# Kernel tuning notes

Measured on AMD Instinct MI355X. Metric: run time of the kernel, lower is better.

Reference implementation:

```python
import jax, jax.numpy as jnp
import numpy as np

H, HKV, D, HID = 64, 8, 64, 2880
T = 2048
WINDOW = 128
THETA = 150000.0
FACTOR = 32.0
ORIG_MAX = 4096
BETA_FAST, BETA_SLOW = 32.0, 1.0
EPS = 1e-5
SCALE = D ** -0.5
MSCALE = float(0.1 * np.log(FACTOR) + 1.0)  # vLLM YaRN attention mscale


def _yarn_inv_freq():
    # vLLM YaRNScalingRotaryEmbedding inverse frequencies
    def corr_dim(n_rot):
        return D * np.log(ORIG_MAX / (n_rot * 2.0 * np.pi)) / (2.0 * np.log(THETA))
    low = max(int(np.floor(corr_dim(BETA_FAST))), 0)
    high = min(int(np.ceil(corr_dim(BETA_SLOW))), D - 1)
    pow_ = np.arange(0, D, 2, dtype=np.float32) / D
    extrap = 1.0 / (THETA ** pow_)                 # extrapolation inv_freq
    interp = extrap / FACTOR                        # interpolation inv_freq
    ramp = np.clip((np.arange(D // 2, dtype=np.float32) - low) / max(high - low, 1e-3), 0.0, 1.0)
    extrap_mask = 1.0 - ramp
    inv_freq = interp * (1.0 - extrap_mask) + extrap * extrap_mask
    return jnp.asarray(inv_freq, jnp.float32)

_INV_FREQ = _yarn_inv_freq()


def _rope(positions, x):
    # neox-style rotation; x: [T, heads, D]
    freqs = positions.astype(jnp.float32)[:, None] * _INV_FREQ[None, :]  # [T, D/2]
    cos = (jnp.cos(freqs) * MSCALE)[:, None, :]
    sin = (jnp.sin(freqs) * MSCALE)[:, None, :]
    x1, x2 = x[..., : D // 2], x[..., D // 2 :]
    return jnp.concatenate([x1 * cos - x2 * sin, x2 * cos + x1 * sin], axis=-1)


def _attn(q, k, v, sinks):
    # q: [T,H,D]; k,v: [T,HKV,D]; sinks: [H] extra softmax logit per head
    g = H // HKV
    k = jnp.repeat(k, g, axis=1)
    v = jnp.repeat(v, g, axis=1)
    scores = jnp.einsum('qhd,khd->hqk', q, k) * SCALE  # [H,T,T]
    i = jnp.arange(T)[:, None]
    j = jnp.arange(T)[None, :]
    mask = (j <= i) & (i - j < WINDOW)  # causal + sliding window (even layer)
    scores = jnp.where(mask[None], scores, -jnp.inf)
    s = sinks[:, None]                                    # [H,1]
    m = jnp.maximum(jnp.max(scores, axis=-1), s)          # [H,T]
    p = jnp.exp(scores - m[..., None])                    # [H,T,T]
    denom = jnp.sum(p, axis=-1) + jnp.exp(s - m)          # sink adds to denominator only
    out = jnp.einsum('hqk,khd->qhd', p, v) / denom.T[..., None]
    return out.reshape(T, H * D)


def setup_inputs() -> dict:
    key = jax.random.key(0)
    ks = jax.random.split(key, 8)
    return {
        'hidden_states': jax.random.normal(ks[0], (T, HID), jnp.float32),
        'positions': jnp.arange(T, dtype=jnp.int32),
        'norm_w': jnp.ones((HID,), jnp.float32),
        'w_qkv': jax.random.normal(ks[1], ((H + 2 * HKV) * D, HID), jnp.float32) * 0.02,
        'b_qkv': jax.random.normal(ks[2], ((H + 2 * HKV) * D,), jnp.float32) * 0.02,
        'w_o': jax.random.normal(ks[3], (HID, H * D), jnp.float32) * 0.02,
        'b_o': jax.random.normal(ks[4], (HID,), jnp.float32) * 0.02,
        'sinks': jax.random.normal(ks[5], (H,), jnp.float32),
    }


def reference(hidden_states, positions, norm_w, w_qkv, b_qkv, w_o, b_o, sinks):
    x = hidden_states
    t = x * jax.lax.rsqrt(jnp.mean(x * x, axis=-1, keepdims=True) + EPS) * norm_w  # RMSNorm
    qkv = t @ w_qkv.T + b_qkv
    q, k, v = jnp.split(qkv, [H * D, H * D + HKV * D], axis=-1)
    q = _rope(positions, q.reshape(T, H, D))
    k = _rope(positions, k.reshape(T, HKV, D))
    v = v.reshape(T, HKV, D)
    attn_out = _attn(q, k, v, sinks)
    out = attn_out @ w_o.T + b_o
    return out + x  # residual
```

## Files before the change

### kernel.cpp

```cpp
#include <hip/hip_runtime.h>
#include <hip/hip_bf16.h>
#include <stdint.h>

typedef __attribute__((ext_vector_type(8))) short bf16x8;
typedef __attribute__((ext_vector_type(4))) float f32x4;
typedef __attribute__((ext_vector_type(4))) unsigned short u16x4;

#define T_SEQ 2048
#define HID_D 2880
#define KPAD 2944
#define NH 64
#define NKV 8
#define HD 64
#define QKV_N 5120
#define ATT_N 4096
#define WIN 128
#define RSCALE 0.125f
#define MSCALE 1.3465735903f

__device__ __forceinline__ unsigned short f2bf(float f) {
  union { float f; unsigned u; } v; v.f = f;
  unsigned r = v.u + 0x7fffu + ((v.u >> 16) & 1u);
  return (unsigned short)(r >> 16);
}

__device__ __forceinline__ void gload_lds16(const void* g, void* l) {
  __builtin_amdgcn_global_load_lds((const __attribute__((address_space(1))) char*)g,
                                   (__attribute__((address_space(3))) char*)l, 16, 0, 0);
}

__global__ __launch_bounds__(256) void rmsnorm_kernel(const float* __restrict__ x,
                                                      const float* __restrict__ w,
                                                      unsigned short* __restrict__ t_bf) {
  int row = blockIdx.x;
  const float4* xr4 = (const float4*)(x + (size_t)row * HID_D);
  const float4* w4 = (const float4*)w;
  float ss = 0.f;
  for (int i = threadIdx.x; i < 720; i += 256) {
    float4 v = xr4[i];
    ss += v.x * v.x + v.y * v.y + v.z * v.z + v.w * v.w;
  }
  __shared__ float red[256];
  red[threadIdx.x] = ss;
  __syncthreads();
  for (int s = 128; s > 0; s >>= 1) {
    if (threadIdx.x < s) red[threadIdx.x] += red[threadIdx.x + s];
    __syncthreads();
  }
  float rs = rsqrtf(red[0] / (float)HID_D + 1e-5f);
  u16x4* ob = (u16x4*)(t_bf + (size_t)row * KPAD);
  for (int i = threadIdx.x; i < 736; i += 256) {
    u16x4 o = {0, 0, 0, 0};
    if (i < 720) {
      float4 v = xr4[i];
      float4 g = w4[i];
      o = { f2bf(v.x * rs * g.x), f2bf(v.y * rs * g.y),
            f2bf(v.z * rs * g.z), f2bf(v.w * rs * g.w) };
    }
    ob[i] = o;
  }
}

__global__ __launch_bounds__(256) void f2bf_pad_kernel(const float* __restrict__ in,
                                                       unsigned short* __restrict__ out,
                                                       int rows, int in4, int out4) {
  int i = blockIdx.x * 256 + threadIdx.x;
  if (i >= rows * out4) return;
  int c4 = i % out4, row = i / out4;
  u16x4 o = {0, 0, 0, 0};
  if (c4 < in4) {
    float4 v = ((const float4*)(in + (size_t)row * in4 * 4))[c4];
    o = { f2bf(v.x), f2bf(v.y), f2bf(v.z), f2bf(v.w) };
  }
  ((u16x4*)out)[(size_t)row * out4 + c4] = o;
}

template <bool NCHECK, bool PARTIAL>
__global__ __launch_bounds__(512, 2) void gemm256p(const unsigned short* __restrict__ A,
                                                   const unsigned short* __restrict__ B,
                                                   float* __restrict__ C,
                                                   const float* __restrict__ bias,
                                                   int M, int N, int ld, int nt,
                                                   int nbx, int nbxy, int nstore) {
  __shared__ unsigned short sA[2 * 2 * 128 * 64];
  __shared__ unsigned short sB[2 * 2 * 128 * 64];

  const int tid = threadIdx.x;
  const int lane = tid & 63, wid = tid >> 6;
  const int wr = wid >> 2, wc = wid & 3;
  const int lq = lane & 15, ro = lane >> 4;

  const int cpx = gridDim.x >> 3;
  const int swz = (blockIdx.x & 7) * cpx + (blockIdx.x >> 3);
  const int kslice = swz / nbxy;
  const int rem = swz - kslice * nbxy;
  const int bx = rem % nbx, by = rem / nbx;
  const int m0 = by * 256, n0 = bx * 256;

  const unsigned short* Ab = A + (size_t)kslice * nt * 64;
  const unsigned short* Bb = B + (size_t)kslice * nt * 64;
  float* Cb = C + (size_t)kslice * M * nstore;

  const int R0 = tid >> 3;
  const int g0 = (((tid & 7) ^ (R0 & 7)) << 3);
  const size_t aOff = (size_t)(m0 + R0) * ld + g0;
  size_t bOff[2][2];
#pragma unroll
  for (int h = 0; h < 2; ++h)
#pragma unroll
    for (int r = 0; r < 2; ++r) {
      int rr = n0 + h * 128 + r * 64 + R0;
      if (NCHECK) rr = min(rr, N - 1);
      bOff[h][r] = (size_t)rr * ld + g0;
    }

  const int ck0 = ((ro ^ (lq & 7)) << 3);
  const int ck1 = (((4 + ro) ^ (lq & 7)) << 3);

#define STG_A(BUF, H, KT)                                                        \
  { unsigned short* _d = sA + ((BUF) * 2 + (H)) * 8192 + wid * 512;              \
    const unsigned short* _s = Ab + aOff + (size_t)((H) * 128) * ld + (KT) * 64; \
    gload_lds16(_s, _d); gload_lds16(_s + (size_t)64 * ld, _d + 4096); }
#define STG_B(BUF, H, KT)                                                        \
  { unsigned short* _d = sB + ((BUF) * 2 + (H)) * 8192 + wid * 512;              \
    gload_lds16(Bb + bOff[H][0] + (KT) * 64, _d);                                \
    gload_lds16(Bb + bOff[H][1] + (KT) * 64, _d + 4096); }

  bf16x8 aR[8];
  bf16x8 bR0[4], bR1[4];
  f32x4 acc[8][4] = {};

#define LDA(BUF, S)                                                                        \
  { _Pragma("unroll") for (int ii = 0; ii < 4; ++ii) {                                     \
      const int _r = ((BUF) * 2 + wr) * 8192 + ((S) * 64 + ii * 16 + lq) * 64;             \
      aR[ii * 2 + 0] = *(const bf16x8*)&sA[_r + ck0];                                      \
      aR[ii * 2 + 1] = *(const bf16x8*)&sA[_r + ck1]; } }
#define LDB(BUF, NHF, DST)                                                                 \
  { _Pragma("unroll") for (int jj = 0; jj < 2; ++jj) {                                     \
      const int _r = ((BUF) * 2 + (wc >> 1)) * 8192 +                                      \
                     ((wc & 1) * 64 + ((NHF) * 2 + jj) * 16 + lq) * 64;                    \
      DST[jj * 2 + 0] = *(const bf16x8*)&sB[_r + ck0];                                     \
      DST[jj * 2 + 1] = *(const bf16x8*)&sB[_r + ck1]; } }
#define MFMA16(S, NHF, BREG)                                                               \
  { _Pragma("unroll") for (int ii = 0; ii < 4; ++ii)                                       \
    _Pragma("unroll") for (int jj = 0; jj < 2; ++jj)                                       \
    _Pragma("unroll") for (int kk = 0; kk < 2; ++kk)                                       \
      acc[(S) * 4 + ii][(NHF) * 2 + jj] = __builtin_amdgcn_mfma_f32_16x16x32_bf16(         \
          aR[ii * 2 + kk], BREG[jj * 2 + kk], acc[(S) * 4 + ii][(NHF) * 2 + jj], 0, 0, 0); }
#define PH_MID()                                         \
  __builtin_amdgcn_s_barrier();                          \
  asm volatile("s_waitcnt lgkmcnt(0)" ::: "memory");     \
  __builtin_amdgcn_sched_barrier(0);                     \
  __builtin_amdgcn_s_setprio(1)
#define PH_END()                                         \
  __builtin_amdgcn_s_setprio(0);                         \
  __builtin_amdgcn_s_barrier()

  STG_A(0, 0, 0); STG_A(0, 1, 0); STG_B(0, 0, 0); STG_B(0, 1, 0);
  STG_B(1, 0, 1); STG_B(1, 1, 1);
  asm volatile("s_waitcnt vmcnt(4)" ::: "memory");
  __builtin_amdgcn_s_barrier();

  const int niter = nt >> 1;
  for (int it = 0; it < niter; ++it) {
    const int t = it * 2;
    const bool more = (it + 1 < niter);
    LDA(0, 0); LDB(0, 0, bR0); STG_A(1, 0, t + 1);
    PH_MID(); MFMA16(0, 0, bR0); PH_END();
    LDB(0, 1, bR1); STG_A(1, 1, t + 1);
    PH_MID(); MFMA16(0, 1, bR1); PH_END();
    LDA(0, 1); if (more) STG_B(0, 0, t + 2);
    PH_MID(); MFMA16(1, 1, bR1); PH_END();
    if (more) STG_B(0, 1, t + 2);
    PH_MID(); MFMA16(1, 0, bR0);
    __builtin_amdgcn_s_setprio(0);
    if (more) asm volatile("s_waitcnt vmcnt(4)" ::: "memory");
    else      asm volatile("s_waitcnt vmcnt(0)" ::: "memory");
    __builtin_amdgcn_s_barrier();
    LDA(1, 0); LDB(1, 0, bR0); if (more) STG_A(0, 0, t + 2);
    PH_MID(); MFMA16(0, 0, bR0); PH_END();
    LDB(1, 1, bR1); if (more) STG_A(0, 1, t + 2);
    PH_MID(); MFMA16(0, 1, bR1); PH_END();
    LDA(1, 1); if (more) STG_B(1, 0, t + 3);
    PH_MID(); MFMA16(1, 1, bR1); PH_END();
    if (more) STG_B(1, 1, t + 3);
    PH_MID(); MFMA16(1, 0, bR0);
    __builtin_amdgcn_s_setprio(0);
    if (more) asm volatile("s_waitcnt vmcnt(4)" ::: "memory");
    else      asm volatile("s_waitcnt vmcnt(0)" ::: "memory");
    __builtin_amdgcn_s_barrier();
  }
#undef STG_A
#undef STG_B
#undef LDA
#undef LDB
#undef MFMA16
#undef PH_MID
#undef PH_END

#pragma unroll
  for (int fi = 0; fi < 8; ++fi) {
    const int gr = m0 + wr * 128 + fi * 16 + ro * 4;
#pragma unroll
    for (int j = 0; j < 4; ++j) {
      const int gc = n0 + wc * 64 + j * 16 + lq;
      if (!NCHECK || gc < N) {
        const float bv = PARTIAL ? 0.0f : bias[gc];
#pragma unroll
        for (int r = 0; r < 4; ++r)
          Cb[(size_t)(gr + r) * nstore + gc] = acc[fi][j][r] + bv;
      }
    }
  }
}

__global__ __launch_bounds__(256) void reduce_out_kernel(const float* __restrict__ part,
                                                         const float* __restrict__ bias,
                                                         const float* __restrict__ x,
                                                         float* __restrict__ out) {
  int i = blockIdx.x * 256 + threadIdx.x;
  if (i >= T_SEQ * 720) return;
  int c4 = i % 720, row = i / 720;
  size_t off = (size_t)row * HID_D + c4 * 4;
  float4 a = *(const float4*)(part + off);
  float4 b = *(const float4*)(part + (size_t)T_SEQ * HID_D + off);
  float4 bv = ((const float4*)bias)[c4];
  float4 xv = *(const float4*)(x + off);
  float4 o = { a.x + b.x + bv.x + xv.x, a.y + b.y + bv.y + xv.y,
               a.z + b.z + bv.z + xv.z, a.w + b.w + bv.w + xv.w };
  *(float4*)(out + off) = o;
}

__global__ __launch_bounds__(256) void rope_kernel(const float* __restrict__ qkv,
                                                   const int* __restrict__ positions,
                                                   unsigned short* __restrict__ qb,
                                                   unsigned short* __restrict__ kb) {
  int idx = blockIdx.x * 256 + threadIdx.x;
  const int total = T_SEQ * (NH + NKV) * 32;
  if (idx >= total) return;
  int d = idx & 31;
  int head = (idx >> 5) % (NH + NKV);
  int t = idx / ((NH + NKV) * 32);
  float pw = (float)d * (1.0f / 32.0f);
  float extrap = expf(-pw * 11.9183905733f);
  float interp = extrap * (1.0f / 32.0f);
  float ramp = fminf(fmaxf(((float)d - 8.0f) * 0.1f, 0.0f), 1.0f);
  float invf = interp * ramp + extrap * (1.0f - ramp);
  float fr = (float)positions[t] * invf;
  float s, c;
  sincosf(fr, &s, &c);
  c *= MSCALE;
  s *= MSCALE;
  if (head < NH) {
    const float* b = qkv + (size_t)t * QKV_N + head * HD + d;
    float x1 = b[0], x2 = b[32];
    unsigned short* ob = qb + (size_t)t * ATT_N + head * HD + d;
    ob[0] = f2bf(x1 * c - x2 * s);
    ob[32] = f2bf(x2 * c + x1 * s);
  } else {
    int gk = head - NH;
    const float* b = qkv + (size_t)t * QKV_N + NH * HD + gk * HD + d;
    float x1 = b[0], x2 = b[32];
    unsigned short* ob = kb + (size_t)t * (NKV * HD) + gk * HD + d;
    ob[0] = f2bf(x1 * c - x2 * s);
    ob[32] = f2bf(x2 * c + x1 * s);
  }
}

__global__ __launch_bounds__(256) void vtrans_kernel(const float* __restrict__ qkv,
                                                     unsigned short* __restrict__ vt) {
  int idx = blockIdx.x * 256 + threadIdx.x;
  int t = idx & (T_SEQ - 1);
  int d = (idx >> 11) & 63;
  int g = idx >> 17;
  vt[idx] = f2bf(qkv[(size_t)t * QKV_N + (NH + NKV) * HD + g * HD + d]);
}

__global__ __launch_bounds__(256) void attn_kernel(const unsigned short* __restrict__ qb,
                                                   const unsigned short* __restrict__ kb,
                                                   const unsigned short* __restrict__ vt,
                                                   const float* __restrict__ sinks,
                                                   unsigned short* __restrict__ att) {
  const int lane = threadIdx.x & 63;
  const int wid = threadIdx.x >> 6;
  const int q0 = blockIdx.x * 16;
  const int h = blockIdx.y * 4 + wid;
  const int g = h >> 3;
  const int lq = lane & 15;
  const int ro = lane >> 4;

  bf16x8 bq0, bq1;
  {
    const unsigned short* qp = qb + (size_t)(q0 + lq) * ATT_N + h * HD + ro * 8;
    bq0 = *(const bf16x8*)qp;
    bq1 = *(const bf16x8*)(qp + 32);
  }
  float m_run = sinks[h];
  float l_run = 1.0f;
  f32x4 o0 = {0.f, 0.f, 0.f, 0.f}, o1 = o0, o2 = o0, o3 = o0;
  const int qg = q0 + lq;
  const int jstart = (q0 >= WIN) ? q0 - WIN : 0;

  for (int jt = jstart; jt <= q0; jt += 32) {
    f32x4 st0 = {0.f, 0.f, 0.f, 0.f}, st1 = st0;
    {
      int kr = jt + ((lq >> 2) << 3) + (lq & 3);
      int kr0 = min(kr, T_SEQ - 1);
      int kr1 = min(kr + 4, T_SEQ - 1);
      const unsigned short* kp0 = kb + (size_t)kr0 * (NKV * HD) + g * HD + ro * 8;
      const unsigned short* kp1 = kb + (size_t)kr1 * (NKV * HD) + g * HD + ro * 8;
      bf16x8 ka0a = *(const bf16x8*)kp0;
      bf16x8 ka0b = *(const bf16x8*)(kp0 + 32);
      bf16x8 ka1a = *(const bf16x8*)kp1;
      bf16x8 ka1b = *(const bf16x8*)(kp1 + 32);
      st0 = __builtin_amdgcn_mfma_f32_16x16x32_bf16(ka0a, bq0, st0, 0, 0, 0);
      st0 = __builtin_amdgcn_mfma_f32_16x16x32_bf16(ka0b, bq1, st0, 0, 0, 0);
      st1 = __builtin_amdgcn_mfma_f32_16x16x32_bf16(ka1a, bq0, st1, 0, 0, 0);
      st1 = __builtin_amdgcn_mfma_f32_16x16x32_bf16(ka1b, bq1, st1, 0, 0, 0);
    }
    float p[8];
    float tmax = -3.0e30f;
#pragma unroll
    for (int r = 0; r < 4; ++r) {
      int jg0 = jt + ro * 8 + r;
      int jg1 = jg0 + 4;
      float s0 = (jg0 <= qg && (qg - jg0) < WIN) ? st0[r] * RSCALE : -3.0e30f;
      float s1 = (jg1 <= qg && (qg - jg1) < WIN) ? st1[r] * RSCALE : -3.0e30f;
      p[r] = s0;
      p[r + 4] = s1;
      tmax = fmaxf(tmax, fmaxf(s0, s1));
    }
    tmax = fmaxf(tmax, __shfl_xor(tmax, 16));
    tmax = fmaxf(tmax, __shfl_xor(tmax, 32));
    float m_new = fmaxf(m_run, tmax);
    float rescale = expf(m_run - m_new);
    float psum = 0.f;
    bf16x8 pa;
#pragma unroll
    for (int jj = 0; jj < 8; ++jj) {
      float pe = expf(p[jj] - m_new);
      psum += pe;
      pa[jj] = (short)f2bf(pe);
    }
    psum += __shfl_xor(psum, 16);
    psum += __shfl_xor(psum, 32);
    l_run = l_run * rescale + psum;
    m_run = m_new;
    f32x4 rs4;
#pragma unroll
    for (int r = 0; r < 4; ++r) rs4[r] = __shfl(rescale, ro * 4 + r);
    o0 *= rs4; o1 *= rs4; o2 *= rs4; o3 *= rs4;
    int tb = jt + ro * 8;
    if (tb > T_SEQ - 8) tb = T_SEQ - 8;
    const unsigned short* vp = vt + (size_t)(g * HD + lq) * T_SEQ + tb;
    bf16x8 v0 = *(const bf16x8*)vp;
    bf16x8 v1 = *(const bf16x8*)(vp + 16 * T_SEQ);
    bf16x8 v2 = *(const bf16x8*)(vp + 32 * T_SEQ);
    bf16x8 v3 = *(const bf16x8*)(vp + 48 * T_SEQ);
    o0 = __builtin_amdgcn_mfma_f32_16x16x32_bf16(pa, v0, o0, 0, 0, 0);
    o1 = __builtin_amdgcn_mfma_f32_16x16x32_bf16(pa, v1, o1, 0, 0, 0);
    o2 = __builtin_amdgcn_mfma_f32_16x16x32_bf16(pa, v2, o2, 0, 0, 0);
    o3 = __builtin_amdgcn_mfma_f32_16x16x32_bf16(pa, v3, o3, 0, 0, 0);
  }

#pragma unroll
  for (int r = 0; r < 4; ++r) {
    float lr = __shfl(l_run, ro * 4 + r);
    float inv = 1.0f / lr;
    int qrow = q0 + ro * 4 + r;
    unsigned short* op = att + (size_t)qrow * ATT_N + h * HD + lq;
    op[0] = f2bf(o0[r] * inv);
    op[16] = f2bf(o1[r] * inv);
    op[32] = f2bf(o2[r] * inv);
    op[48] = f2bf(o3[r] * inv);
  }
}

extern "C" void kernel_launch(void* const* d_in, const int* in_sizes, int n_in,
                              void* d_out, int out_size, void* d_ws, size_t ws_size,
                              hipStream_t stream) {
  const float* x = (const float*)d_in[0];
  const int* pos = (const int*)d_in[1];
  const float* norm_w = (const float*)d_in[2];
  const float* w_qkv = (const float*)d_in[3];
  const float* b_qkv = (const float*)d_in[4];
  const float* w_o = (const float*)d_in[5];
  const float* b_o = (const float*)d_in[6];
  const float* sinks = (const float*)d_in[7];
  float* out = (float*)d_out;

  unsigned short* t_bf = (unsigned short*)d_ws;
  unsigned short* wq_bf = t_bf + (size_t)T_SEQ * KPAD;
  unsigned short* wo_bf = wq_bf + (size_t)QKV_N * KPAD;
  float* qkv = (float*)(wo_bf + (size_t)HID_D * ATT_N);
  unsigned short* qb = (unsigned short*)(qkv + (size_t)T_SEQ * QKV_N);
  unsigned short* kb = qb + (size_t)T_SEQ * ATT_N;
  unsigned short* vt = kb + (size_t)T_SEQ * NKV * HD;
  unsigned short* att = vt + (size_t)NKV * HD * T_SEQ;
  float* part = qkv;

  rmsnorm_kernel<<<T_SEQ, 256, 0, stream>>>(x, norm_w, t_bf);
  f2bf_pad_kernel<<<(QKV_N * 736 + 255) / 256, 256, 0, stream>>>(w_qkv, wq_bf, QKV_N, 720, 736);
  f2bf_pad_kernel<<<(HID_D * 1024 + 255) / 256, 256, 0, stream>>>(w_o, wo_bf, HID_D, 1024, 1024);
  gemm256p<false, false><<<160, 512, 0, stream>>>(
      t_bf, wq_bf, qkv, b_qkv, T_SEQ, QKV_N, KPAD, 46, 20, 160, QKV_N);
  rope_kernel<<<(T_SEQ * (NH + NKV) * 32 + 255) / 256, 256, 0, stream>>>(qkv, pos, qb, kb);
  vtrans_kernel<<<(NKV * HD * T_SEQ) / 256, 256, 0, stream>>>(qkv, vt);
  attn_kernel<<<dim3(T_SEQ / 16, NH / 4), 256, 0, stream>>>(qb, kb, vt, sinks, att);
  gemm256p<true, true><<<192, 512, 0, stream>>>(
      att, wo_bf, part, b_o, T_SEQ, HID_D, ATT_N, 32, 12, 96, HID_D);
  reduce_out_kernel<<<(T_SEQ * 720 + 255) / 256, 256, 0, stream>>>(part, b_o, x, out);
}
```

Before: 265.1 us.

## Merge prep kernels, overlap w_o conversion with QKV GEMM, emit bf16 QKV

```diff
diff --git a/kernel.cpp b/kernel.cpp
--- a/kernel.cpp
+++ b/kernel.cpp
@@ -17,81 +17,86 @@
 #define WIN 128
 #define RSCALE 0.125f
 #define MSCALE 1.3465735903f
+#define ROPE_TOT (T_SEQ * (NH + NKV) * 32)
+#define VT_TOT (NKV * HD * T_SEQ)
 
 __device__ __forceinline__ unsigned short f2bf(float f) {
   union { float f; unsigned u; } v; v.f = f;
   unsigned r = v.u + 0x7fffu + ((v.u >> 16) & 1u);
   return (unsigned short)(r >> 16);
 }
+__device__ __forceinline__ float bf2f(unsigned short u) {
+  union { unsigned u; float f; } v; v.u = ((unsigned)u) << 16;
+  return v.f;
+}
 
 __device__ __forceinline__ void gload_lds16(const void* g, void* l) {
   __builtin_amdgcn_global_load_lds((const __attribute__((address_space(1))) char*)g,
                                    (__attribute__((address_space(3))) char*)l, 16, 0, 0);
 }
 
-__global__ __launch_bounds__(256) void rmsnorm_kernel(const float* __restrict__ x,
-                                                      const float* __restrict__ w,
-                                                      unsigned short* __restrict__ t_bf) {
-  int row = blockIdx.x;
-  const float4* xr4 = (const float4*)(x + (size_t)row * HID_D);
-  const float4* w4 = (const float4*)w;
-  float ss = 0.f;
-  for (int i = threadIdx.x; i < 720; i += 256) {
-    float4 v = xr4[i];
-    ss += v.x * v.x + v.y * v.y + v.z * v.z + v.w * v.w;
-  }
+__global__ __launch_bounds__(256) void pre_kernel(const float* __restrict__ x,
+                                                  const float* __restrict__ w,
+                                                  unsigned short* __restrict__ t_bf,
+                                                  const float* __restrict__ wq_src,
+                                                  unsigned short* __restrict__ wq_dst) {
   __shared__ float red[256];
-  red[threadIdx.x] = ss;
-  __syncthreads();
-  for (int s = 128; s > 0; s >>= 1) {
-    if (threadIdx.x < s) red[threadIdx.x] += red[threadIdx.x + s];
+  if (blockIdx.x < 2048) {
+    int row = blockIdx.x;
+    const float4* xr4 = (const float4*)(x + (size_t)row * HID_D);
+    const float4* w4 = (const float4*)w;
+    float ss = 0.f;
+    for (int i = threadIdx.x; i < 720; i += 256) {
+      float4 v = xr4[i];
+      ss += v.x * v.x + v.y * v.y + v.z * v.z + v.w * v.w;
+    }
+    red[threadIdx.x] = ss;
     __syncthreads();
-  }
-  float rs = rsqrtf(red[0] / (float)HID_D + 1e-5f);
-  u16x4* ob = (u16x4*)(t_bf + (size_t)row * KPAD);
-  for (int i = threadIdx.x; i < 736; i += 256) {
-    u16x4 o = {0, 0, 0, 0};
-    if (i < 720) {
-      float4 v = xr4[i];
-      float4 g = w4[i];
-      o = { f2bf(v.x * rs * g.x), f2bf(v.y * rs * g.y),
-            f2bf(v.z * rs * g.z), f2bf(v.w * rs * g.w) };
-    }
-    ob[i] = o;
-  }
-}
-
-__global__ __launch_bounds__(256) void f2bf_pad_kernel(const float* __restrict__ in,
-                                                       unsigned short* __restrict__ out,
-                                                       int rows, int in4, int out4) {
-  int i = blockIdx.x * 256 + threadIdx.x;
-  if (i >= rows * out4) return;
-  int c4 = i % out4, row = i / out4;
-  u16x4 o = {0, 0, 0, 0};
-  if (c4 < in4) {
-    float4 v = ((const float4*)(in + (size_t)row * in4 * 4))[c4];
-    o = { f2bf(v.x), f2bf(v.y), f2bf(v.z), f2bf(v.w) };
-  }
-  ((u16x4*)out)[(size_t)row * out4 + c4] = o;
-}
-
-template <bool NCHECK, bool PARTIAL>
-__global__ __launch_bounds__(512, 2) void gemm256p(const unsigned short* __restrict__ A,
-                                                   const unsigned short* __restrict__ B,
-                                                   float* __restrict__ C,
-                                                   const float* __restrict__ bias,
-                                                   int M, int N, int ld, int nt,
-                                                   int nbx, int nbxy, int nstore) {
-  __shared__ unsigned short sA[2 * 2 * 128 * 64];
-  __shared__ unsigned short sB[2 * 2 * 128 * 64];
-
+    for (int s = 128; s > 0; s >>= 1) {
+      if (threadIdx.x < s) red[threadIdx.x] += red[threadIdx.x + s];
+      __syncthreads();
+    }
+    float rs = rsqrtf(red[0] / (float)HID_D + 1e-5f);
+    u16x4* ob = (u16x4*)(t_bf + (size_t)row * KPAD);
+    for (int i = threadIdx.x; i < 736; i += 256) {
+      u16x4 o = {0, 0, 0, 0};
+      if (i < 720) {
+        float4 v = xr4[i];
+        float4 g = w4[i];
+        o = { f2bf(v.x * rs * g.x), f2bf(v.y * rs * g.y),
+              f2bf(v.z * rs * g.z), f2bf(v.w * rs * g.w) };
+      }
+      ob[i] = o;
+    }
+  } else {
+    const int total = QKV_N * 736;
+    for (int i = (blockIdx.x - 2048) * 256 + threadIdx.x; i < total; i += 1024 * 256) {
+      int c4 = i % 736, row = i / 736;
+      u16x4 o = {0, 0, 0, 0};
+      if (c4 < 720) {
+        float4 v = ((const float4*)wq_src)[(size_t)row * 720 + c4];
+        o = { f2bf(v.x), f2bf(v.y), f2bf(v.z), f2bf(v.w) };
+      }
+      ((u16x4*)wq_dst)[i] = o;
+    }
+  }
+}
+
+template <bool NCHECK, int MODE>
+__device__ __forceinline__ void gemm_body(const unsigned short* __restrict__ A,
+                                          const unsigned short* __restrict__ B,
+                                          void* __restrict__ C0,
+                                          float* __restrict__ Cpart,
+                                          const float* __restrict__ bias,
+                                          const float* __restrict__ resid,
+                                          int M, int N, int ld, int nt,
+                                          int nbx, int nbxy, int nstore, int swz,
+                                          unsigned short* sA, unsigned short* sB) {
   const int tid = threadIdx.x;
   const int lane = tid & 63, wid = tid >> 6;
   const int wr = wid >> 2, wc = wid & 3;
   const int lq = lane & 15, ro = lane >> 4;
 
-  const int cpx = gridDim.x >> 3;
-  const int swz = (blockIdx.x & 7) * cpx + (blockIdx.x >> 3);
   const int kslice = swz / nbxy;
   const int rem = swz - kslice * nbxy;
   const int bx = rem % nbx, by = rem / nbx;
@@ -99,7 +104,6 @@
 
   const unsigned short* Ab = A + (size_t)kslice * nt * 64;
   const unsigned short* Bb = B + (size_t)kslice * nt * 64;
-  float* Cb = C + (size_t)kslice * M * nstore;
 
   const int R0 = tid >> 3;
   const int g0 = (((tid & 7) ^ (R0 & 7)) << 3);
@@ -205,75 +209,119 @@
     for (int j = 0; j < 4; ++j) {
       const int gc = n0 + wc * 64 + j * 16 + lq;
       if (!NCHECK || gc < N) {
-        const float bv = PARTIAL ? 0.0f : bias[gc];
-#pragma unroll
-        for (int r = 0; r < 4; ++r)
-          Cb[(size_t)(gr + r) * nstore + gc] = acc[fi][j][r] + bv;
+        if (MODE == 2) {
+          const float bv = bias[gc];
+          unsigned short* Cs = (unsigned short*)C0;
+#pragma unroll
+          for (int r = 0; r < 4; ++r)
+            Cs[(size_t)(gr + r) * nstore + gc] = f2bf(acc[fi][j][r] + bv);
+        } else {
+          if (kslice == 0) {
+            float* Cf = (float*)C0;
+            const float bv = bias[gc];
+#pragma unroll
+            for (int r = 0; r < 4; ++r) {
+              size_t off = (size_t)(gr + r) * nstore + gc;
+              Cf[off] = acc[fi][j][r] + bv + resid[off];
+            }
+          } else {
+#pragma unroll
+            for (int r = 0; r < 4; ++r)
+              Cpart[(size_t)(gr + r) * nstore + gc] = acc[fi][j][r];
+          }
+        }
       }
     }
   }
 }
 
-__global__ __launch_bounds__(256) void reduce_out_kernel(const float* __restrict__ part,
-                                                         const float* __restrict__ bias,
-                                                         const float* __restrict__ x,
-                                                         float* __restrict__ out) {
+__global__ __launch_bounds__(512, 2) void qkv_fused_kernel(const unsigned short* __restrict__ A,
+                                                           const unsigned short* __restrict__ B,
+                                                           unsigned short* __restrict__ C,
+                                                           const float* __restrict__ bias,
+                                                           const float* __restrict__ wo_src,
+                                                           unsigned short* __restrict__ wo_dst) {
+  __shared__ unsigned short sA[2 * 2 * 128 * 64];
+  __shared__ unsigned short sB[2 * 2 * 128 * 64];
+  const int c = blockIdx.x & 7, q = blockIdx.x >> 3;
+  if (q < 20) {
+    gemm_body<false, 2>(A, B, C, nullptr, bias, nullptr,
+                        T_SEQ, QKV_N, KPAD, 46, 20, 160, QKV_N, c * 20 + q, sA, sB);
+  } else {
+    const int cid = c * 12 + (q - 20);
+    const int total = HID_D * 1024;
+    for (int i = cid * 512 + threadIdx.x; i < total; i += 96 * 512) {
+      float4 v = ((const float4*)wo_src)[i];
+      u16x4 o = { f2bf(v.x), f2bf(v.y), f2bf(v.z), f2bf(v.w) };
+      ((u16x4*)wo_dst)[i] = o;
+    }
+  }
+}
+
+__global__ __launch_bounds__(512, 2) void outproj_kernel(const unsigned short* __restrict__ att,
+                                                         const unsigned short* __restrict__ wo_bf,
+                                                         float* __restrict__ out,
+                                                         float* __restrict__ part,
+                                                         const float* __restrict__ b_o,
+                                                         const float* __restrict__ x) {
+  __shared__ unsigned short sA[2 * 2 * 128 * 64];
+  __shared__ unsigned short sB[2 * 2 * 128 * 64];
+  const int swz = (blockIdx.x & 7) * 24 + (blockIdx.x >> 3);
+  gemm_body<true, 1>(att, wo_bf, out, part, b_o, x,
+                     T_SEQ, HID_D, ATT_N, 32, 12, 96, HID_D, swz, sA, sB);
+}
+
+__global__ __launch_bounds__(256) void reduce_add_kernel(float* __restrict__ out,
+                                                         const float* __restrict__ part) {
   int i = blockIdx.x * 256 + threadIdx.x;
   if (i >= T_SEQ * 720) return;
-  int c4 = i % 720, row = i / 720;
-  size_t off = (size_t)row * HID_D + c4 * 4;
-  float4 a = *(const float4*)(part + off);
-  float4 b = *(const float4*)(part + (size_t)T_SEQ * HID_D + off);
-  float4 bv = ((const float4*)bias)[c4];
-  float4 xv = *(const float4*)(x + off);
-  float4 o = { a.x + b.x + bv.x + xv.x, a.y + b.y + bv.y + xv.y,
-               a.z + b.z + bv.z + xv.z, a.w + b.w + bv.w + xv.w };
-  *(float4*)(out + off) = o;
-}
-
-__global__ __launch_bounds__(256) void rope_kernel(const float* __restrict__ qkv,
-                                                   const int* __restrict__ positions,
-                                                   unsigned short* __restrict__ qb,
-                                                   unsigned short* __restrict__ kb) {
+  float4 o = ((const float4*)out)[i];
+  float4 p = ((const float4*)part)[i];
+  o.x += p.x; o.y += p.y; o.z += p.z; o.w += p.w;
+  ((float4*)out)[i] = o;
+}
+
+__global__ __launch_bounds__(256) void ropev_kernel(const unsigned short* __restrict__ qkvb,
+                                                    const int* __restrict__ positions,
+                                                    unsigned short* __restrict__ qb,
+                                                    unsigned short* __restrict__ kb,
+                                                    unsigned short* __restrict__ vt) {
   int idx = blockIdx.x * 256 + threadIdx.x;
-  const int total = T_SEQ * (NH + NKV) * 32;
-  if (idx >= total) return;
-  int d = idx & 31;
-  int head = (idx >> 5) % (NH + NKV);
-  int t = idx / ((NH + NKV) * 32);
-  float pw = (float)d * (1.0f / 32.0f);
-  float extrap = expf(-pw * 11.9183905733f);
-  float interp = extrap * (1.0f / 32.0f);
-  float ramp = fminf(fmaxf(((float)d - 8.0f) * 0.1f, 0.0f), 1.0f);
-  float invf = interp * ramp + extrap * (1.0f - ramp);
-  float fr = (float)positions[t] * invf;
-  float s, c;
-  sincosf(fr, &s, &c);
-  c *= MSCALE;
-  s *= MSCALE;
-  if (head < NH) {
-    const float* b = qkv + (size_t)t * QKV_N + head * HD + d;
-    float x1 = b[0], x2 = b[32];
-    unsigned short* ob = qb + (size_t)t * ATT_N + head * HD + d;
-    ob[0] = f2bf(x1 * c - x2 * s);
-    ob[32] = f2bf(x2 * c + x1 * s);
+  if (idx < ROPE_TOT) {
+    int d = idx & 31;
+    int head = (idx >> 5) % (NH + NKV);
+    int t = idx / ((NH + NKV) * 32);
+    float pw = (float)d * (1.0f / 32.0f);
+    float extrap = expf(-pw * 11.9183905733f);
+    float interp = extrap * (1.0f / 32.0f);
+    float ramp = fminf(fmaxf(((float)d - 8.0f) * 0.1f, 0.0f), 1.0f);
+    float invf = interp * ramp + extrap * (1.0f - ramp);
+    float fr = (float)positions[t] * invf;
+    float s, c;
+    sincosf(fr, &s, &c);
+    c *= MSCALE;
+    s *= MSCALE;
+    if (head < NH) {
+      const unsigned short* b = qkvb + (size_t)t * QKV_N + head * HD + d;
+      float x1 = bf2f(b[0]), x2 = bf2f(b[32]);
+      unsigned short* ob = qb + (size_t)t * ATT_N + head * HD + d;
+      ob[0] = f2bf(x1 * c - x2 * s);
+      ob[32] = f2bf(x2 * c + x1 * s);
+    } else {
+      int gk = head - NH;
+      const unsigned short* b = qkvb + (size_t)t * QKV_N + NH * HD + gk * HD + d;
+      float x1 = bf2f(b[0]), x2 = bf2f(b[32]);
+      unsigned short* ob = kb + (size_t)t * (NKV * HD) + gk * HD + d;
+      ob[0] = f2bf(x1 * c - x2 * s);
+      ob[32] = f2bf(x2 * c + x1 * s);
+    }
   } else {
-    int gk = head - NH;
-    const float* b = qkv + (size_t)t * QKV_N + NH * HD + gk * HD + d;
-    float x1 = b[0], x2 = b[32];
-    unsigned short* ob = kb + (size_t)t * (NKV * HD) + gk * HD + d;
-    ob[0] = f2bf(x1 * c - x2 * s);
-    ob[32] = f2bf(x2 * c + x1 * s);
-  }
-}
-
-__global__ __launch_bounds__(256) void vtrans_kernel(const float* __restrict__ qkv,
-                                                     unsigned short* __restrict__ vt) {
-  int idx = blockIdx.x * 256 + threadIdx.x;
-  int t = idx & (T_SEQ - 1);
-  int d = (idx >> 11) & 63;
-  int g = idx >> 17;
-  vt[idx] = f2bf(qkv[(size_t)t * QKV_N + (NH + NKV) * HD + g * HD + d]);
+    int i2 = idx - ROPE_TOT;
+    int t = i2 & (T_SEQ - 1);
+    int d = (i2 >> 11) & 63;
+    int g = i2 >> 17;
+    vt[i2] = qkvb[(size_t)t * QKV_N + (NH + NKV) * HD + g * HD + d];
+  }
 }
 
 __global__ __launch_bounds__(256) void attn_kernel(const unsigned short* __restrict__ qb,
@@ -392,22 +440,17 @@
   unsigned short* t_bf = (unsigned short*)d_ws;
   unsigned short* wq_bf = t_bf + (size_t)T_SEQ * KPAD;
   unsigned short* wo_bf = wq_bf + (size_t)QKV_N * KPAD;
-  float* qkv = (float*)(wo_bf + (size_t)HID_D * ATT_N);
-  unsigned short* qb = (unsigned short*)(qkv + (size_t)T_SEQ * QKV_N);
+  unsigned short* qkv_bf = wo_bf + (size_t)HID_D * ATT_N;
+  unsigned short* qb = qkv_bf + (size_t)T_SEQ * QKV_N;
   unsigned short* kb = qb + (size_t)T_SEQ * ATT_N;
   unsigned short* vt = kb + (size_t)T_SEQ * NKV * HD;
   unsigned short* att = vt + (size_t)NKV * HD * T_SEQ;
-  float* part = qkv;
-
-  rmsnorm_kernel<<<T_SEQ, 256, 0, stream>>>(x, norm_w, t_bf);
-  f2bf_pad_kernel<<<(QKV_N * 736 + 255) / 256, 256, 0, stream>>>(w_qkv, wq_bf, QKV_N, 720, 736);
-  f2bf_pad_kernel<<<(HID_D * 1024 + 255) / 256, 256, 0, stream>>>(w_o, wo_bf, HID_D, 1024, 1024);
-  gemm256p<false, false><<<160, 512, 0, stream>>>(
-      t_bf, wq_bf, qkv, b_qkv, T_SEQ, QKV_N, KPAD, 46, 20, 160, QKV_N);
-  rope_kernel<<<(T_SEQ * (NH + NKV) * 32 + 255) / 256, 256, 0, stream>>>(qkv, pos, qb, kb);
-  vtrans_kernel<<<(NKV * HD * T_SEQ) / 256, 256, 0, stream>>>(qkv, vt);
+  float* part = (float*)d_ws;
+
+  pre_kernel<<<3072, 256, 0, stream>>>(x, norm_w, t_bf, w_qkv, wq_bf);
+  qkv_fused_kernel<<<256, 512, 0, stream>>>(t_bf, wq_bf, qkv_bf, b_qkv, w_o, wo_bf);
+  ropev_kernel<<<(ROPE_TOT + VT_TOT) / 256, 256, 0, stream>>>(qkv_bf, pos, qb, kb, vt);
   attn_kernel<<<dim3(T_SEQ / 16, NH / 4), 256, 0, stream>>>(qb, kb, vt, sinks, att);
-  gemm256p<true, true><<<192, 512, 0, stream>>>(
-      att, wo_bf, part, b_o, T_SEQ, HID_D, ATT_N, 32, 12, 96, HID_D);
-  reduce_out_kernel<<<(T_SEQ * 720 + 255) / 256, 256, 0, stream>>>(part, b_o, x, out);
-}
+  outproj_kernel<<<192, 512, 0, stream>>>(att, wo_bf, out, part, b_o, x);
+  reduce_add_kernel<<<(T_SEQ * 720 + 255) / 256, 256, 0, stream>>>(out, part);
+}
```

New measurement: 252.7 us. 1.05x faster.
